# Kernel optimization log

Measured on AMD Instinct MI355X. Metric: run time of the kernel, lower is better.

The kernel has to match this reference:

```python
import jax, jax.numpy as jnp
import numpy as np
from jax import lax

B, L, P, CIN, N, HD, PH, K = 2048, 96, 96, 8, 64, 64, 8, 3
DIM_C = CIN * N  # 512


def _silu(x):
    return x * jax.nn.sigmoid(x)


def _lin(x, w, b):
    return x @ w.T + b


def setup_inputs() -> dict:
    key = jax.random.key(0)
    ks = iter(jax.random.split(key, 64))

    def w(shape):
        fan_in = shape[-1]
        return (jax.random.normal(next(ks), shape, jnp.float32) / np.sqrt(fan_in)).astype(jnp.float32)

    inp = {"x": jax.random.normal(next(ks), (B, L, CIN), jnp.float32)}
    # x_proj: 5 Linears (enc_in->h, h->h, h->h, h->h, h->N), SiLU between (dropout=eval/identity)
    inp["xp_w0"] = w((HD, CIN)); inp["xp_b0"] = jnp.zeros((HD,), jnp.float32)
    inp["xp_w1"] = w((HD, HD));  inp["xp_b1"] = jnp.zeros((HD,), jnp.float32)
    inp["xp_w2"] = w((HD, HD));  inp["xp_b2"] = jnp.zeros((HD,), jnp.float32)
    inp["xp_w3"] = w((HD, HD));  inp["xp_b3"] = jnp.zeros((HD,), jnp.float32)
    inp["xp_w4"] = w((N, HD));   inp["xp_b4"] = jnp.zeros((N,), jnp.float32)
    # x_proj_: Linear(N,h), SiLU, Linear(h,N)
    inp["xpp_w0"] = w((HD, N)); inp["xpp_b0"] = jnp.zeros((HD,), jnp.float32)
    inp["xpp_w1"] = w((N, HD)); inp["xpp_b1"] = jnp.zeros((N,), jnp.float32)
    # depthwise dilated Conv1d: weight (N, 1, K)
    inp["conv_w"] = w((N, 1, K)); inp["conv_b"] = jnp.zeros((N,), jnp.float32)
    inp["span_A"] = jnp.asarray(0.1, jnp.float32)
    # compress: Linear(N*L, PH)
    inp["comp_w"] = w((PH, N * L)); inp["comp_b"] = jnp.zeros((PH,), jnp.float32)
    # a_ode.net: Linear(PH,h), SiLU, Linear(h,PH), Tanh
    inp["net_w0"] = w((HD, PH)); inp["net_b0"] = jnp.zeros((HD,), jnp.float32)
    inp["net_w1"] = w((PH, HD)); inp["net_b1"] = jnp.zeros((PH,), jnp.float32)
    # lat2out: Linear(PH,8), SiLU, Linear(8,N)
    inp["lo_w0"] = w((8, PH)); inp["lo_b0"] = jnp.zeros((8,), jnp.float32)
    inp["lo_w1"] = w((N, 8));  inp["lo_b1"] = jnp.zeros((N,), jnp.float32)
    # lat2out_c: Linear(PH,8), SiLU, Linear(8, CIN*N)
    inp["lc_w0"] = w((8, PH));     inp["lc_b0"] = jnp.zeros((8,), jnp.float32)
    inp["lc_w1"] = w((DIM_C, 8));  inp["lc_b1"] = jnp.zeros((DIM_C,), jnp.float32)
    # lat2out_z: Linear(N,N), SiLU, Linear(N, CIN)
    inp["lz_w0"] = w((N, N));   inp["lz_b0"] = jnp.zeros((N,), jnp.float32)
    inp["lz_w1"] = w((CIN, N)); inp["lz_b1"] = jnp.zeros((CIN,), jnp.float32)
    return inp


def reference(x, xp_w0, xp_b0, xp_w1, xp_b1, xp_w2, xp_b2, xp_w3, xp_b3, xp_w4, xp_b4,
              xpp_w0, xpp_b0, xpp_w1, xpp_b1, conv_w, conv_b, span_A, comp_w, comp_b,
              net_w0, net_b0, net_w1, net_b1, lo_w0, lo_b0, lo_w1, lo_b1,
              lc_w0, lc_b0, lc_w1, lc_b1, lz_w0, lz_b0, lz_w1, lz_b1):
    Bsz = x.shape[0]

    def x_proj(t):
        h = _silu(_lin(t, xp_w0, xp_b0))
        h = _silu(_lin(h, xp_w1, xp_b1))
        h = _silu(_lin(h, xp_w2, xp_b2))
        h = _silu(_lin(h, xp_w3, xp_b3))
        return _lin(h, xp_w4, xp_b4)

    x_old = x_proj(x[:, :L])                       # (B, L, N)
    hist = x_old.transpose(0, 2, 1)                # (B, N, L)
    pad = (K - 1) * 2                              # 4
    conv = lax.conv_general_dilated(
        hist, conv_w, window_strides=(1,), padding=[(pad, pad)],
        rhs_dilation=(2,), dimension_numbers=("NCH", "OIH", "NCH"),
        feature_group_count=N) + conv_b[None, :, None]
    hist = _silu(conv)[:, :, -L:]                  # (B, N, L)
    hist_f = hist.transpose(0, 2, 1).reshape(Bsz, L * N)
    vector_F = _lin(hist_f, comp_w, comp_b)        # (B, PH)

    a0 = vector_F
    z0 = x_proj(x[:, L - 1])                       # (B, N)

    # Householder matrix H = I - 2 v v^T with v = normalize(x_proj_(z0))
    v = _lin(_silu(_lin(z0, xpp_w0, xpp_b0)), xpp_w1, xpp_b1)
    v = v / (jnp.linalg.norm(v, axis=-1, keepdims=True) + 1e-8)
    Hh = jnp.eye(N, dtype=x.dtype)[None] - 2.0 * v[:, :, None] * v[:, None, :]  # (B,N,N)

    dt = jnp.clip(span_A, 1e-8, 7.0)               # uniform Euler step size
    s0 = jnp.concatenate([a0, z0], axis=-1)        # (B, PH+N)

    def step(s, _):
        a = s[:, :PH]
        z = s[:, PH:]
        da = jnp.tanh(_lin(_silu(_lin(a, net_w0, net_b0)), net_w1, net_b1))  # (B,PH)
        d = _lin(_silu(_lin(a, lo_w0, lo_b0)), lo_w1, lo_b1)                 # (B,N)
        # dz = H^T diag(d) H z   (fused; avoids materializing A_mat)
        Hz = jnp.einsum('bjk,bk->bj', Hh, z)
        dz = jnp.einsum('bj,bji->bi', d * Hz, Hh)
        s_new = s + dt * jnp.concatenate([da, dz], axis=-1)
        return s_new, s_new

    _, sol = lax.scan(step, s0, None, length=P)    # (P, B, PH+N) == sol[1:]

    c_traj = sol[:, :, :PH]                        # (P, B, PH)
    z_traj = sol[:, :, PH:]                        # (P, B, N)

    C = _lin(_silu(_lin(c_traj, lc_w0, lc_b0)), lc_w1, lc_b1)  # (P, B, CIN*N)
    C = C.reshape(P, Bsz, CIN, N)
    y_hat_c = jnp.einsum('pbcn,pbn->pbc', C, z_traj)           # (P, B, CIN)
    added_z = _lin(_silu(_lin(z_traj, lz_w0, lz_b0)), lz_w1, lz_b1)
    x_pred = (y_hat_c + added_z).transpose(1, 0, 2)            # (B, P, CIN)

    x_rec = x[:, :L, :]
    return (x_rec, x_pred)
```

## Files before the change

kernel.cpp:

```cpp
#include <hip/hip_runtime.h>
#include <cstdint>
#include <cstddef>

#define BB 2048
#define LL 96
#define PP 96
#define NN 64
#define HSTRIDE 68
#define RSTR 84

typedef __attribute__((ext_vector_type(8))) short short8;
typedef __attribute__((ext_vector_type(4))) float f32x4;

union U4S8 { uint4 u; short8 s; };

__device__ __forceinline__ float siluf(float x) {
  return x * __builtin_amdgcn_rcpf(1.0f + __expf(-x));
}
__device__ __forceinline__ float tanhf_fast(float x) {
  return 1.0f - 2.0f * __builtin_amdgcn_rcpf(1.0f + __expf(2.0f * x));
}
__device__ __forceinline__ float rlane(float x, int l) {
  return __int_as_float(__builtin_amdgcn_readlane(__float_as_int(x), l));
}

__device__ __forceinline__ uint32_t packsplit(float f) {
  uint32_t b = __float_as_uint(f);
  uint32_t h = b & 0xFFFF0000u;
  float r = f - __uint_as_float(h);
  return h | (__float_as_uint(r) >> 16);
}
__device__ __forceinline__ void splitpack2(float f0, float f1, uint32_t& dhi, uint32_t& dlo) {
  uint32_t b0 = __float_as_uint(f0), b1 = __float_as_uint(f1);
  uint32_t h0 = b0 & 0xFFFF0000u, h1 = b1 & 0xFFFF0000u;
  float r0 = f0 - __uint_as_float(h0), r1 = f1 - __uint_as_float(h1);
  dhi = (h0 >> 16) | h1;
  dlo = (__float_as_uint(r0) >> 16) | (__float_as_uint(r1) & 0xFFFF0000u);
}
__device__ __forceinline__ void unpack2(uint32_t p0, uint32_t p1, uint32_t& dhi, uint32_t& dlo) {
  dhi = (p0 >> 16) | (p1 & 0xFFFF0000u);
  dlo = (p0 & 0xFFFFu) | (p1 << 16);
}
__device__ __forceinline__ void readfrag(const uint32_t* p, short8& hi, short8& lo) {
  uint4 pa = *(const uint4*)p;
  uint4 pb = *(const uint4*)(p + 4);
  U4S8 h, l;
  unpack2(pa.x, pa.y, h.u.x, l.u.x);
  unpack2(pa.z, pa.w, h.u.y, l.u.y);
  unpack2(pb.x, pb.y, h.u.z, l.u.z);
  unpack2(pb.z, pb.w, h.u.w, l.u.w);
  hi = h.s; lo = l.s;
}
__device__ __forceinline__ f32x4 mm_split(f32x4 acc, const short8* Ah, const short8* Al,
                                          const short8* Bh, const short8* Bl) {
  acc = __builtin_amdgcn_mfma_f32_16x16x32_bf16(Ah[0], Bh[0], acc, 0, 0, 0);
  acc = __builtin_amdgcn_mfma_f32_16x16x32_bf16(Ah[1], Bh[1], acc, 0, 0, 0);
  acc = __builtin_amdgcn_mfma_f32_16x16x32_bf16(Al[0], Bh[0], acc, 0, 0, 0);
  acc = __builtin_amdgcn_mfma_f32_16x16x32_bf16(Al[1], Bh[1], acc, 0, 0, 0);
  acc = __builtin_amdgcn_mfma_f32_16x16x32_bf16(Ah[0], Bl[0], acc, 0, 0, 0);
  acc = __builtin_amdgcn_mfma_f32_16x16x32_bf16(Ah[1], Bl[1], acc, 0, 0, 0);
  return acc;
}

__global__ __launch_bounds__(256, 2) void k_xproj(
    const float* __restrict__ x,
    const float* __restrict__ w0, const float* __restrict__ b0,
    const float* __restrict__ w1, const float* __restrict__ b1,
    const float* __restrict__ w2, const float* __restrict__ b2,
    const float* __restrict__ w3, const float* __restrict__ b3,
    const float* __restrict__ w4, const float* __restrict__ b4,
    float* __restrict__ x_old, float* __restrict__ out)
{
  __shared__ uint32_t hbuf[128 * HSTRIDE];
  __shared__ uint32_t wbuf[64 * HSTRIDE];
  __shared__ float bs[320];

  int tid = threadIdx.x;
  int wave = tid >> 6, lane = tid & 63;
  int quad = lane >> 4, m16 = lane & 15;
  size_t tokBase = (size_t)blockIdx.x * 128;

  {
    size_t e = tokBase * 8 + (size_t)tid * 4;
    *(float4*)(out + e) = *(const float4*)(x + e);
  }
  if (tid < 64) {
    bs[tid]       = b0[tid];
    bs[64 + tid]  = b1[tid];
    bs[128 + tid] = b2[tid];
    bs[192 + tid] = b3[tid];
    bs[256 + tid] = b4[tid];
  }
  __syncthreads();

  short8 A0h[2], A0l[2];
  #pragma unroll
  for (int mt = 0; mt < 2; ++mt) {
    U4S8 h, l;
    h.u = make_uint4(0, 0, 0, 0); l.u = make_uint4(0, 0, 0, 0);
    if (quad == 0) {
      const float* xp = x + (tokBase + wave * 32 + mt * 16 + m16) * 8;
      float4 xa = *(const float4*)xp;
      float4 xb = *(const float4*)(xp + 4);
      splitpack2(xa.x, xa.y, h.u.x, l.u.x);
      splitpack2(xa.z, xa.w, h.u.y, l.u.y);
      splitpack2(xb.x, xb.y, h.u.z, l.u.z);
      splitpack2(xb.z, xb.w, h.u.w, l.u.w);
    }
    A0h[mt] = h.s; A0l[mt] = l.s;
  }
  short8 B0h[4], B0l[4];
  #pragma unroll
  for (int nt = 0; nt < 4; ++nt) {
    U4S8 h, l;
    h.u = make_uint4(0, 0, 0, 0); l.u = make_uint4(0, 0, 0, 0);
    if (quad == 0) {
      const float* wp = w0 + (nt * 16 + m16) * 8;
      float4 wa = *(const float4*)wp;
      float4 wb = *(const float4*)(wp + 4);
      splitpack2(wa.x, wa.y, h.u.x, l.u.x);
      splitpack2(wa.z, wa.w, h.u.y, l.u.y);
      splitpack2(wb.x, wb.y, h.u.z, l.u.z);
      splitpack2(wb.z, wb.w, h.u.w, l.u.w);
    }
    B0h[nt] = h.s; B0l[nt] = l.s;
  }
  {
    f32x4 acc[2][4];
    #pragma unroll
    for (int mt = 0; mt < 2; ++mt)
      #pragma unroll
      for (int nt = 0; nt < 4; ++nt) {
        float bv = bs[nt * 16 + m16];
        acc[mt][nt] = (f32x4){bv, bv, bv, bv};
      }
    #pragma unroll
    for (int mt = 0; mt < 2; ++mt)
      #pragma unroll
      for (int nt = 0; nt < 4; ++nt)
        acc[mt][nt] = __builtin_amdgcn_mfma_f32_16x16x32_bf16(A0h[mt], B0h[nt], acc[mt][nt], 0, 0, 0);
    #pragma unroll
    for (int mt = 0; mt < 2; ++mt)
      #pragma unroll
      for (int nt = 0; nt < 4; ++nt)
        acc[mt][nt] = __builtin_amdgcn_mfma_f32_16x16x32_bf16(A0l[mt], B0h[nt], acc[mt][nt], 0, 0, 0);
    #pragma unroll
    for (int mt = 0; mt < 2; ++mt)
      #pragma unroll
      for (int nt = 0; nt < 4; ++nt)
        acc[mt][nt] = __builtin_amdgcn_mfma_f32_16x16x32_bf16(A0h[mt], B0l[nt], acc[mt][nt], 0, 0, 0);
    #pragma unroll
    for (int mt = 0; mt < 2; ++mt)
      #pragma unroll
      for (int nt = 0; nt < 4; ++nt)
        #pragma unroll
        for (int r = 0; r < 4; ++r) {
          float s = siluf(acc[mt][nt][r]);
          hbuf[(wave * 32 + mt * 16 + quad * 4 + r) * HSTRIDE + nt * 16 + m16] = packsplit(s);
        }
  }

  const float* Ws[4] = {w1, w2, w3, w4};
  #pragma unroll 1
  for (int lyr = 0; lyr < 4; ++lyr) {
    const float* w = Ws[lyr];
    #pragma unroll
    for (int i = 0; i < 4; ++i) {
      int e4 = i * 256 + tid;
      int o = e4 >> 4, k = (e4 & 15) << 2;
      float4 wv = ((const float4*)w)[e4];
      *(uint4*)(wbuf + o * HSTRIDE + k) =
          make_uint4(packsplit(wv.x), packsplit(wv.y), packsplit(wv.z), packsplit(wv.w));
    }
    __syncthreads();
    short8 Bh[8], Bl[8];
    #pragma unroll
    for (int nt = 0; nt < 4; ++nt)
      #pragma unroll
      for (int ks = 0; ks < 2; ++ks)
        readfrag(wbuf + (nt * 16 + m16) * HSTRIDE + ks * 32 + quad * 8, Bh[nt * 2 + ks], Bl[nt * 2 + ks]);
    short8 Ah[4], Al[4];
    #pragma unroll
    for (int mt = 0; mt < 2; ++mt)
      #pragma unroll
      for (int ks = 0; ks < 2; ++ks)
        readfrag(hbuf + (wave * 32 + mt * 16 + m16) * HSTRIDE + ks * 32 + quad * 8, Ah[mt * 2 + ks], Al[mt * 2 + ks]);
    __syncthreads();

    f32x4 acc[2][4];
    #pragma unroll
    for (int mt = 0; mt < 2; ++mt)
      #pragma unroll
      for (int nt = 0; nt < 4; ++nt) {
        float bv = bs[(lyr + 1) * 64 + nt * 16 + m16];
        acc[mt][nt] = (f32x4){bv, bv, bv, bv};
      }
    #pragma unroll
    for (int ks = 0; ks < 2; ++ks)
      #pragma unroll
      for (int mt = 0; mt < 2; ++mt)
        #pragma unroll
        for (int nt = 0; nt < 4; ++nt)
          acc[mt][nt] = __builtin_amdgcn_mfma_f32_16x16x32_bf16(Ah[mt * 2 + ks], Bh[nt * 2 + ks], acc[mt][nt], 0, 0, 0);
    #pragma unroll
    for (int ks = 0; ks < 2; ++ks)
      #pragma unroll
      for (int mt = 0; mt < 2; ++mt)
        #pragma unroll
        for (int nt = 0; nt < 4; ++nt)
          acc[mt][nt] = __builtin_amdgcn_mfma_f32_16x16x32_bf16(Al[mt * 2 + ks], Bh[nt * 2 + ks], acc[mt][nt], 0, 0, 0);
    #pragma unroll
    for (int ks = 0; ks < 2; ++ks)
      #pragma unroll
      for (int mt = 0; mt < 2; ++mt)
        #pragma unroll
        for (int nt = 0; nt < 4; ++nt)
          acc[mt][nt] = __builtin_amdgcn_mfma_f32_16x16x32_bf16(Ah[mt * 2 + ks], Bl[nt * 2 + ks], acc[mt][nt], 0, 0, 0);

    if (lyr < 3) {
      #pragma unroll
      for (int mt = 0; mt < 2; ++mt)
        #pragma unroll
        for (int nt = 0; nt < 4; ++nt)
          #pragma unroll
          for (int r = 0; r < 4; ++r) {
            float s = siluf(acc[mt][nt][r]);
            hbuf[(wave * 32 + mt * 16 + quad * 4 + r) * HSTRIDE + nt * 16 + m16] = packsplit(s);
          }
    } else {
      #pragma unroll
      for (int mt = 0; mt < 2; ++mt)
        #pragma unroll
        for (int nt = 0; nt < 4; ++nt)
          #pragma unroll
          for (int r = 0; r < 4; ++r) {
            size_t t = tokBase + wave * 32 + mt * 16 + quad * 4 + r;
            x_old[t * 64 + nt * 16 + m16] = acc[mt][nt][r];
          }
    }
  }
}

__global__ __launch_bounds__(256) void k_hist(
    const float* __restrict__ x_old,
    const float* __restrict__ conv_w, const float* __restrict__ conv_b,
    const float* __restrict__ comp_w, const float* __restrict__ comp_b,
    const float* __restrict__ xw0, const float* __restrict__ xb0,
    const float* __restrict__ xw1, const float* __restrict__ xb1,
    float* __restrict__ a0_o, float* __restrict__ v_o, float* __restrict__ z0_o)
{
  __shared__ float xo[LL * NN];
  __shared__ float red[32];
  __shared__ float hbuf[64];
  int b = blockIdx.x, tid = threadIdx.x;
  const float* src = x_old + (size_t)b * (LL * NN);
  #pragma unroll
  for (int i = 0; i < 6; ++i) {
    int e = (i * 256 + tid) * 4;
    *(float4*)(xo + e) = *(const float4*)(src + e);
  }
  __syncthreads();
  int c = tid & 63;
  float cw0 = conv_w[c * 3], cw1 = conv_w[c * 3 + 1], cw2 = conv_w[c * 3 + 2];
  float cb = conv_b[c];
  float acc[8];
  #pragma unroll
  for (int q = 0; q < 8; ++q) acc[q] = 0.f;
  #pragma unroll 1
  for (int j = 0; j < 24; ++j) {
    int e = j * 256 + tid;
    int t = e >> 6;
    float s = xo[t * 64 + c] * cw0 + cb;
    if (t + 2 < LL) s += xo[(t + 2) * 64 + c] * cw1;
    if (t + 4 < LL) s += xo[(t + 4) * 64 + c] * cw2;
    float hv = siluf(s);
    #pragma unroll
    for (int q = 0; q < 8; ++q) acc[q] += hv * comp_w[q * 6144 + e];
  }
  #pragma unroll
  for (int off = 32; off >= 1; off >>= 1) {
    #pragma unroll
    for (int q = 0; q < 8; ++q) acc[q] += __shfl_xor(acc[q], off, 64);
  }
  int wave = tid >> 6, lane = tid & 63;
  if (lane < 8) {
    float sel = acc[0];
    #pragma unroll
    for (int q = 1; q < 8; ++q) sel = (lane == q) ? acc[q] : sel;
    red[wave * 8 + lane] = sel;
  }
  __syncthreads();
  if (tid < 8)
    a0_o[b * 8 + tid] = red[tid] + red[8 + tid] + red[16 + tid] + red[24 + tid] + comp_b[tid];
  if (tid < 64) {
    float a2 = xb0[tid];
    #pragma unroll 8
    for (int k = 0; k < 64; ++k) a2 += xw0[tid * 64 + k] * xo[6080 + k];
    hbuf[tid] = siluf(a2);
  }
  __syncthreads();
  float vr = 0.f;
  if (tid < 64) {
    vr = xb1[tid];
    #pragma unroll 8
    for (int k = 0; k < 64; ++k) vr += xw1[tid * 64 + k] * hbuf[k];
  }
  float s2 = vr * vr;
  #pragma unroll
  for (int off = 32; off >= 1; off >>= 1) s2 += __shfl_xor(s2, off, 64);
  if (tid < 64) {
    float nrm = sqrtf(s2) + 1e-8f;
    v_o[b * 64 + tid] = vr / nrm;
    z0_o[b * 64 + tid] = xo[6080 + tid];
  }
}

__global__ __launch_bounds__(256) void k_scan(
    const float* __restrict__ a0_i, const float* __restrict__ v_i, const float* __restrict__ z0_i,
    const float* __restrict__ nw0, const float* __restrict__ nb0_p,
    const float* __restrict__ nw1, const float* __restrict__ nb1_p,
    const float* __restrict__ lw0, const float* __restrict__ lb0_p,
    const float* __restrict__ lw1, const float* __restrict__ lb1_p,
    const float* __restrict__ spanA, float* __restrict__ atraj, float* __restrict__ ztraj)
{
  int lane = threadIdx.x & 63;
  int b = blockIdx.x * 4 + (threadIdx.x >> 6);
  float dt = fminf(fmaxf(spanA[0], 1e-8f), 7.0f);
  int i8 = lane & 7;
  float w0r[8], w1r[8], g0r[8], d1r[8];
  #pragma unroll
  for (int i = 0; i < 8; ++i) w0r[i] = nw0[lane * 8 + i];
  #pragma unroll
  for (int i = 0; i < 8; ++i) w1r[i] = nw1[i * 64 + lane];
  #pragma unroll
  for (int i = 0; i < 8; ++i) g0r[i] = lw0[i8 * 8 + i];
  #pragma unroll
  for (int i = 0; i < 8; ++i) d1r[i] = lw1[lane * 8 + i];
  float nb0 = nb0_p[lane];
  float nb1o = nb1_p[i8];
  float lb0o = lb0_p[i8];
  float lb1 = lb1_p[lane];
  float v = v_i[b * 64 + lane];
  float z = z0_i[b * 64 + lane];
  float a_own = a0_i[b * 8 + i8];
  float t0 = v * z;
  #pragma unroll
  for (int off = 32; off >= 1; off >>= 1) t0 += __shfl_xor(t0, off, 64);
  float w = z - 2.0f * t0 * v;
  float a_s[8];
  #pragma unroll
  for (int i = 0; i < 8; ++i) a_s[i] = rlane(a_own, i);

  float* ab = atraj + (size_t)b * (PP * 8);
  float* zb = ztraj + (size_t)b * (PP * NN);
  #pragma unroll 1
  for (int p = 0; p < PP; ++p) {
    float h = nb0;
    #pragma unroll
    for (int i = 0; i < 8; ++i) h += w0r[i] * a_s[i];
    h = siluf(h);
    float pr[8];
    #pragma unroll
    for (int i = 0; i < 8; ++i) pr[i] = w1r[i] * h;
    #pragma unroll
    for (int off = 1; off <= 4; off <<= 1) {
      #pragma unroll
      for (int i = 0; i < 8; ++i) pr[i] += __shfl_xor(pr[i], off, 64);
    }
    float ps = pr[0];
    #pragma unroll
    for (int i = 1; i < 8; ++i) ps = (i8 == i) ? pr[i] : ps;
    ps += __shfl_xor(ps, 8, 64);
    ps += __shfl_xor(ps, 16, 64);
    ps += __shfl_xor(ps, 32, 64);
    float da_own = tanhf_fast(ps + nb1o);
    float ga = lb0o;
    #pragma unroll
    for (int i = 0; i < 8; ++i) ga += g0r[i] * a_s[i];
    float g_own = siluf(ga);
    float d = lb1;
    #pragma unroll
    for (int j = 0; j < 8; ++j) d += d1r[j] * rlane(g_own, j);
    a_own += dt * da_own;
    #pragma unroll
    for (int i = 0; i < 8; ++i) a_s[i] = rlane(a_own, i);
    w *= (1.0f + dt * d);
    float t1 = v * w;
    #pragma unroll
    for (int off = 32; off >= 1; off >>= 1) t1 += __shfl_xor(t1, off, 64);
    float zv = w - 2.0f * t1 * v;
    if (lane < 8) ab[p * 8 + lane] = a_own;
    zb[p * 64 + lane] = zv;
  }
}

__global__ __launch_bounds__(256, 2) void k_post(
    const float* __restrict__ atraj, const float* __restrict__ ztraj,
    const float* __restrict__ cw0, const float* __restrict__ cb0,
    const float* __restrict__ cw1, const float* __restrict__ cb1,
    const float* __restrict__ zw0, const float* __restrict__ zb0,
    const float* __restrict__ zw1, const float* __restrict__ zb1,
    float* __restrict__ out)
{
  __shared__ uint32_t zbuf[64 * HSTRIDE];
  __shared__ uint32_t wbuf[80 * HSTRIDE];
  __shared__ float    resbuf[64 * RSTR];
  __shared__ float    cw0s[64];
  __shared__ float    cb0s[8];
  __shared__ float    zb0s[64];
  __shared__ float    zb1s[8];

  int tid = threadIdx.x;
  int wave = tid >> 6, lane = tid & 63;
  int quad = lane >> 4, m16 = lane & 15;
  size_t tokBase = (size_t)blockIdx.x * 64;

  #pragma unroll
  for (int i = 0; i < 4; ++i) {
    int e4 = i * 256 + tid;
    int t = e4 >> 4, k = (e4 & 15) << 2;
    float4 zv = *(const float4*)(ztraj + (tokBase + t) * 64 + k);
    *(uint4*)(zbuf + t * HSTRIDE + k) =
        make_uint4(packsplit(zv.x), packsplit(zv.y), packsplit(zv.z), packsplit(zv.w));
  }
  #pragma unroll
  for (int i = 0; i < 20; ++i) {
    int e = i * 256 + tid;
    int o = e >> 6, k = e & 63;
    float wv;
    if (o < 64)       wv = cw1[(((o >> 3) * 64 + k) << 3) + (o & 7)];
    else if (o < 72)  wv = cb1[(o - 64) * 64 + k];
    else              wv = 0.f;
    wbuf[o * HSTRIDE + k] = packsplit(wv);
  }
  if (tid < 64) cw0s[tid] = cw0[tid];
  if (tid < 8)  cb0s[tid] = cb0[tid];
  if (tid < 64) zb0s[tid] = zb0[tid];
  if (tid < 8)  zb1s[tid] = zb1[tid];
  __syncthreads();

  short8 Ah[2], Al[2];
  readfrag(zbuf + (wave * 16 + m16) * HSTRIDE + quad * 8,      Ah[0], Al[0]);
  readfrag(zbuf + (wave * 16 + m16) * HSTRIDE + 32 + quad * 8, Ah[1], Al[1]);

  #pragma unroll
  for (int nt = 0; nt < 5; ++nt) {
    short8 Bh[2], Bl[2];
    readfrag(wbuf + (nt * 16 + m16) * HSTRIDE + quad * 8,      Bh[0], Bl[0]);
    readfrag(wbuf + (nt * 16 + m16) * HSTRIDE + 32 + quad * 8, Bh[1], Bl[1]);
    f32x4 acc = (f32x4){0.f, 0.f, 0.f, 0.f};
    acc = mm_split(acc, Ah, Al, Bh, Bl);
    int o = nt * 16 + m16;
    if (o < 72) {
      #pragma unroll
      for (int r = 0; r < 4; ++r)
        resbuf[(wave * 16 + quad * 4 + r) * RSTR + o] = acc[r];
    }
  }
  __syncthreads();

  #pragma unroll
  for (int i = 0; i < 16; ++i) {
    int e = i * 256 + tid;
    int o = e >> 6, k = e & 63;
    wbuf[o * HSTRIDE + k] = packsplit(zw0[o * 64 + k]);
  }
  __syncthreads();

  #pragma unroll
  for (int nt = 0; nt < 4; ++nt) {
    short8 Bh[2], Bl[2];
    readfrag(wbuf + (nt * 16 + m16) * HSTRIDE + quad * 8,      Bh[0], Bl[0]);
    readfrag(wbuf + (nt * 16 + m16) * HSTRIDE + 32 + quad * 8, Bh[1], Bl[1]);
    f32x4 acc = (f32x4){0.f, 0.f, 0.f, 0.f};
    acc = mm_split(acc, Ah, Al, Bh, Bl);
    int m = nt * 16 + m16;
    float zb = zb0s[m];
    #pragma unroll
    for (int r = 0; r < 4; ++r) {
      float e = siluf(acc[r] + zb);
      zbuf[(wave * 16 + quad * 4 + r) * HSTRIDE + m] = packsplit(e);
    }
  }
  __syncthreads();

  #pragma unroll
  for (int i = 0; i < 4; ++i) {
    int e = i * 256 + tid;
    int o = e >> 6, k = e & 63;
    wbuf[o * HSTRIDE + k] = (o < 8) ? packsplit(zw1[o * 64 + k]) : 0u;
  }
  __syncthreads();

  {
    short8 Eh[2], El[2];
    readfrag(zbuf + (wave * 16 + m16) * HSTRIDE + quad * 8,      Eh[0], El[0]);
    readfrag(zbuf + (wave * 16 + m16) * HSTRIDE + 32 + quad * 8, Eh[1], El[1]);
    short8 Bh[2], Bl[2];
    readfrag(wbuf + m16 * HSTRIDE + quad * 8,      Bh[0], Bl[0]);
    readfrag(wbuf + m16 * HSTRIDE + 32 + quad * 8, Bh[1], Bl[1]);
    f32x4 acc = (f32x4){0.f, 0.f, 0.f, 0.f};
    acc = mm_split(acc, Eh, El, Bh, Bl);
    if (m16 < 8) {
      float zb = zb1s[m16];
      #pragma unroll
      for (int r = 0; r < 4; ++r)
        resbuf[(wave * 16 + quad * 4 + r) * RSTR + 72 + m16] = acc[r] + zb;
    }
  }
  __syncthreads();

  if (tid < 64) {
    size_t idx = tokBase + tid;
    const float* ap = atraj + idx * 8;
    float4 a0v = *(const float4*)ap;
    float4 a1v = *(const float4*)(ap + 4);
    float a[8] = {a0v.x, a0v.y, a0v.z, a0v.w, a1v.x, a1v.y, a1v.z, a1v.w};
    float g2[8];
    #pragma unroll
    for (int j = 0; j < 8; ++j) {
      float t = cb0s[j];
      #pragma unroll
      for (int i = 0; i < 8; ++i) t += cw0s[j * 8 + i] * a[i];
      g2[j] = siluf(t);
    }
    const float* rr = resbuf + tid * RSTR;
    float yc[8];
    #pragma unroll
    for (int c = 0; c < 8; ++c) {
      float y = rr[64 + c] + rr[72 + c];
      #pragma unroll
      for (int j = 0; j < 8; ++j) y += rr[c * 8 + j] * g2[j];
      yc[c] = y;
    }
    float* op = out + (size_t)(BB * LL * 8) + idx * 8;
    *(float4*)op       = make_float4(yc[0], yc[1], yc[2], yc[3]);
    *(float4*)(op + 4) = make_float4(yc[4], yc[5], yc[6], yc[7]);
  }
}

extern "C" void kernel_launch(void* const* d_in, const int* in_sizes, int n_in,
                              void* d_out, int out_size, void* d_ws, size_t ws_size,
                              hipStream_t stream) {
  const float* x      = (const float*)d_in[0];
  const float* xp_w0  = (const float*)d_in[1];
  const float* xp_b0  = (const float*)d_in[2];
  const float* xp_w1  = (const float*)d_in[3];
  const float* xp_b1  = (const float*)d_in[4];
  const float* xp_w2  = (const float*)d_in[5];
  const float* xp_b2  = (const float*)d_in[6];
  const float* xp_w3  = (const float*)d_in[7];
  const float* xp_b3  = (const float*)d_in[8];
  const float* xp_w4  = (const float*)d_in[9];
  const float* xp_b4  = (const float*)d_in[10];
  const float* xpp_w0 = (const float*)d_in[11];
  const float* xpp_b0 = (const float*)d_in[12];
  const float* xpp_w1 = (const float*)d_in[13];
  const float* xpp_b1 = (const float*)d_in[14];
  const float* conv_w = (const float*)d_in[15];
  const float* conv_b = (const float*)d_in[16];
  const float* span_A = (const float*)d_in[17];
  const float* comp_w = (const float*)d_in[18];
  const float* comp_b = (const float*)d_in[19];
  const float* net_w0 = (const float*)d_in[20];
  const float* net_b0 = (const float*)d_in[21];
  const float* net_w1 = (const float*)d_in[22];
  const float* net_b1 = (const float*)d_in[23];
  const float* lo_w0  = (const float*)d_in[24];
  const float* lo_b0  = (const float*)d_in[25];
  const float* lo_w1  = (const float*)d_in[26];
  const float* lo_b1  = (const float*)d_in[27];
  const float* lc_w0  = (const float*)d_in[28];
  const float* lc_b0  = (const float*)d_in[29];
  const float* lc_w1  = (const float*)d_in[30];
  const float* lc_b1  = (const float*)d_in[31];
  const float* lz_w0  = (const float*)d_in[32];
  const float* lz_b0  = (const float*)d_in[33];
  const float* lz_w1  = (const float*)d_in[34];
  const float* lz_b1  = (const float*)d_in[35];

  float* ws    = (float*)d_ws;
  float* x_old = ws;
  float* ztraj = ws;
  float* atraj = ws + 12582912;
  float* a0    = ws + 14155776;
  float* vv    = a0 + 2048 * 8;
  float* z0    = vv + 2048 * 64;
  float* out   = (float*)d_out;

  hipLaunchKernelGGL(k_xproj, dim3(1536), dim3(256), 0, stream,
                     x, xp_w0, xp_b0, xp_w1, xp_b1, xp_w2, xp_b2, xp_w3, xp_b3,
                     xp_w4, xp_b4, x_old, out);
  hipLaunchKernelGGL(k_hist, dim3(2048), dim3(256), 0, stream,
                     x_old, conv_w, conv_b, comp_w, comp_b,
                     xpp_w0, xpp_b0, xpp_w1, xpp_b1, a0, vv, z0);
  hipLaunchKernelGGL(k_scan, dim3(512), dim3(256), 0, stream,
                     a0, vv, z0, net_w0, net_b0, net_w1, net_b1,
                     lo_w0, lo_b0, lo_w1, lo_b1, span_A, atraj, ztraj);
  hipLaunchKernelGGL(k_post, dim3(3072), dim3(256), 0, stream,
                     atraj, ztraj, lc_w0, lc_b0, lc_w1, lc_b1,
                     lz_w0, lz_b0, lz_w1, lz_b1, out);
}
```

Measured before the change: 361.4 us.

## Pre-split z trajectory in scan, preload all post weights, LDS-based da reduction

The scan kernel now writes z trajectory values already packed into the hi/lo split format, and computes the net_w1 product by staging h in shared memory instead of a shuffle-heavy 8-way reduction. The post kernel reads A fragments directly from global memory, loads all of its weight matrices into one larger LDS buffer up front (removing several barriers and reload phases), and spreads the final output computation over all 256 threads. The result buffer stride also changes. The aim is fewer syncs, less conversion work and fewer shuffles. The cost is more LDS per block, which may reduce occupancy.

```diff
diff --git a/kernel.cpp b/kernel.cpp
--- a/kernel.cpp
+++ b/kernel.cpp
@@ -7,7 +7,7 @@
 #define PP 96
 #define NN 64
 #define HSTRIDE 68
-#define RSTR 84
+#define RSTR 81
 
 typedef __attribute__((ext_vector_type(8))) short short8;
 typedef __attribute__((ext_vector_type(4))) float f32x4;
@@ -321,17 +321,23 @@
     const float* __restrict__ nw1, const float* __restrict__ nb1_p,
     const float* __restrict__ lw0, const float* __restrict__ lb0_p,
     const float* __restrict__ lw1, const float* __restrict__ lb1_p,
-    const float* __restrict__ spanA, float* __restrict__ atraj, float* __restrict__ ztraj)
+    const float* __restrict__ spanA, float* __restrict__ atraj, uint32_t* __restrict__ ztraj)
 {
-  int lane = threadIdx.x & 63;
-  int b = blockIdx.x * 4 + (threadIdx.x >> 6);
+  __shared__ float hshm[4 * 72];
+  int tid = threadIdx.x;
+  int lane = tid & 63;
+  int wv = tid >> 6;
+  int b = blockIdx.x * 4 + wv;
   float dt = fminf(fmaxf(spanA[0], 1e-8f), 7.0f);
   int i8 = lane & 7;
-  float w0r[8], w1r[8], g0r[8], d1r[8];
+  int oct = lane >> 3;
+  float* hs = hshm + wv * 72;
+
+  float w0r[8], w1L[8], g0r[8], d1r[8];
   #pragma unroll
   for (int i = 0; i < 8; ++i) w0r[i] = nw0[lane * 8 + i];
   #pragma unroll
-  for (int i = 0; i < 8; ++i) w1r[i] = nw1[i * 64 + lane];
+  for (int j = 0; j < 8; ++j) w1L[j] = nw1[i8 * 64 + oct * 8 + j];
   #pragma unroll
   for (int i = 0; i < 8; ++i) g0r[i] = lw0[i8 * 8 + i];
   #pragma unroll
@@ -352,28 +358,22 @@
   for (int i = 0; i < 8; ++i) a_s[i] = rlane(a_own, i);
 
   float* ab = atraj + (size_t)b * (PP * 8);
-  float* zb = ztraj + (size_t)b * (PP * NN);
+  uint32_t* zb = ztraj + (size_t)b * (PP * NN);
   #pragma unroll 1
   for (int p = 0; p < PP; ++p) {
     float h = nb0;
     #pragma unroll
     for (int i = 0; i < 8; ++i) h += w0r[i] * a_s[i];
     h = siluf(h);
-    float pr[8];
-    #pragma unroll
-    for (int i = 0; i < 8; ++i) pr[i] = w1r[i] * h;
-    #pragma unroll
-    for (int off = 1; off <= 4; off <<= 1) {
-      #pragma unroll
-      for (int i = 0; i < 8; ++i) pr[i] += __shfl_xor(pr[i], off, 64);
-    }
-    float ps = pr[0];
-    #pragma unroll
-    for (int i = 1; i < 8; ++i) ps = (i8 == i) ? pr[i] : ps;
-    ps += __shfl_xor(ps, 8, 64);
-    ps += __shfl_xor(ps, 16, 64);
-    ps += __shfl_xor(ps, 32, 64);
-    float da_own = tanhf_fast(ps + nb1o);
+    hs[lane] = h;
+    float4 h0 = *(const float4*)(hs + oct * 8);
+    float4 h1 = *(const float4*)(hs + oct * 8 + 4);
+    float psum = w1L[0] * h0.x + w1L[1] * h0.y + w1L[2] * h0.z + w1L[3] * h0.w
+               + w1L[4] * h1.x + w1L[5] * h1.y + w1L[6] * h1.z + w1L[7] * h1.w;
+    psum += __shfl_xor(psum, 8, 64);
+    psum += __shfl_xor(psum, 16, 64);
+    psum += __shfl_xor(psum, 32, 64);
+    float da_own = tanhf_fast(psum + nb1o);
     float ga = lb0o;
     #pragma unroll
     for (int i = 0; i < 8; ++i) ga += g0r[i] * a_s[i];
@@ -390,20 +390,20 @@
     for (int off = 32; off >= 1; off >>= 1) t1 += __shfl_xor(t1, off, 64);
     float zv = w - 2.0f * t1 * v;
     if (lane < 8) ab[p * 8 + lane] = a_own;
-    zb[p * 64 + lane] = zv;
+    zb[p * 64 + lane] = packsplit(zv);
   }
 }
 
 __global__ __launch_bounds__(256, 2) void k_post(
-    const float* __restrict__ atraj, const float* __restrict__ ztraj,
+    const float* __restrict__ atraj, const uint32_t* __restrict__ ztraj,
     const float* __restrict__ cw0, const float* __restrict__ cb0,
     const float* __restrict__ cw1, const float* __restrict__ cb1,
     const float* __restrict__ zw0, const float* __restrict__ zb0,
     const float* __restrict__ zw1, const float* __restrict__ zb1,
     float* __restrict__ out)
 {
-  __shared__ uint32_t zbuf[64 * HSTRIDE];
-  __shared__ uint32_t wbuf[80 * HSTRIDE];
+  __shared__ uint32_t wbuf[144 * HSTRIDE];
+  __shared__ uint32_t ebuf[64 * HSTRIDE];
   __shared__ float    resbuf[64 * RSTR];
   __shared__ float    cw0s[64];
   __shared__ float    cb0s[8];
@@ -416,21 +416,14 @@
   size_t tokBase = (size_t)blockIdx.x * 64;
 
   #pragma unroll
-  for (int i = 0; i < 4; ++i) {
-    int e4 = i * 256 + tid;
-    int t = e4 >> 4, k = (e4 & 15) << 2;
-    float4 zv = *(const float4*)(ztraj + (tokBase + t) * 64 + k);
-    *(uint4*)(zbuf + t * HSTRIDE + k) =
-        make_uint4(packsplit(zv.x), packsplit(zv.y), packsplit(zv.z), packsplit(zv.w));
-  }
-  #pragma unroll
-  for (int i = 0; i < 20; ++i) {
+  for (int i = 0; i < 36; ++i) {
     int e = i * 256 + tid;
     int o = e >> 6, k = e & 63;
     float wv;
     if (o < 64)       wv = cw1[(((o >> 3) * 64 + k) << 3) + (o & 7)];
     else if (o < 72)  wv = cb1[(o - 64) * 64 + k];
-    else              wv = 0.f;
+    else if (o < 136) wv = zw0[(o - 72) * 64 + k];
+    else              wv = zw1[(o - 136) * 64 + k];
     wbuf[o * HSTRIDE + k] = packsplit(wv);
   }
   if (tid < 64) cw0s[tid] = cw0[tid];
@@ -439,9 +432,10 @@
   if (tid < 8)  zb1s[tid] = zb1[tid];
   __syncthreads();
 
+  const uint32_t* zp = ztraj + (tokBase + wave * 16 + m16) * 64;
   short8 Ah[2], Al[2];
-  readfrag(zbuf + (wave * 16 + m16) * HSTRIDE + quad * 8,      Ah[0], Al[0]);
-  readfrag(zbuf + (wave * 16 + m16) * HSTRIDE + 32 + quad * 8, Ah[1], Al[1]);
+  readfrag(zp + quad * 8,      Ah[0], Al[0]);
+  readfrag(zp + 32 + quad * 8, Ah[1], Al[1]);
 
   #pragma unroll
   for (int nt = 0; nt < 5; ++nt) {
@@ -457,61 +451,45 @@
         resbuf[(wave * 16 + quad * 4 + r) * RSTR + o] = acc[r];
     }
   }
-  __syncthreads();
-
-  #pragma unroll
-  for (int i = 0; i < 16; ++i) {
-    int e = i * 256 + tid;
-    int o = e >> 6, k = e & 63;
-    wbuf[o * HSTRIDE + k] = packsplit(zw0[o * 64 + k]);
-  }
-  __syncthreads();
 
   #pragma unroll
   for (int nt = 0; nt < 4; ++nt) {
     short8 Bh[2], Bl[2];
-    readfrag(wbuf + (nt * 16 + m16) * HSTRIDE + quad * 8,      Bh[0], Bl[0]);
-    readfrag(wbuf + (nt * 16 + m16) * HSTRIDE + 32 + quad * 8, Bh[1], Bl[1]);
+    readfrag(wbuf + (72 + nt * 16 + m16) * HSTRIDE + quad * 8,      Bh[0], Bl[0]);
+    readfrag(wbuf + (72 + nt * 16 + m16) * HSTRIDE + 32 + quad * 8, Bh[1], Bl[1]);
     f32x4 acc = (f32x4){0.f, 0.f, 0.f, 0.f};
     acc = mm_split(acc, Ah, Al, Bh, Bl);
     int m = nt * 16 + m16;
-    float zb = zb0s[m];
+    float zbv = zb0s[m];
     #pragma unroll
     for (int r = 0; r < 4; ++r) {
-      float e = siluf(acc[r] + zb);
-      zbuf[(wave * 16 + quad * 4 + r) * HSTRIDE + m] = packsplit(e);
-    }
-  }
-  __syncthreads();
-
-  #pragma unroll
-  for (int i = 0; i < 4; ++i) {
-    int e = i * 256 + tid;
-    int o = e >> 6, k = e & 63;
-    wbuf[o * HSTRIDE + k] = (o < 8) ? packsplit(zw1[o * 64 + k]) : 0u;
-  }
-  __syncthreads();
+      float e = siluf(acc[r] + zbv);
+      ebuf[(wave * 16 + quad * 4 + r) * HSTRIDE + m] = packsplit(e);
+    }
+  }
 
   {
     short8 Eh[2], El[2];
-    readfrag(zbuf + (wave * 16 + m16) * HSTRIDE + quad * 8,      Eh[0], El[0]);
-    readfrag(zbuf + (wave * 16 + m16) * HSTRIDE + 32 + quad * 8, Eh[1], El[1]);
+    readfrag(ebuf + (wave * 16 + m16) * HSTRIDE + quad * 8,      Eh[0], El[0]);
+    readfrag(ebuf + (wave * 16 + m16) * HSTRIDE + 32 + quad * 8, Eh[1], El[1]);
     short8 Bh[2], Bl[2];
-    readfrag(wbuf + m16 * HSTRIDE + quad * 8,      Bh[0], Bl[0]);
-    readfrag(wbuf + m16 * HSTRIDE + 32 + quad * 8, Bh[1], Bl[1]);
+    int brow = 136 + (m16 & 7);
+    readfrag(wbuf + brow * HSTRIDE + quad * 8,      Bh[0], Bl[0]);
+    readfrag(wbuf + brow * HSTRIDE + 32 + quad * 8, Bh[1], Bl[1]);
     f32x4 acc = (f32x4){0.f, 0.f, 0.f, 0.f};
     acc = mm_split(acc, Eh, El, Bh, Bl);
     if (m16 < 8) {
-      float zb = zb1s[m16];
+      float zbv = zb1s[m16];
       #pragma unroll
       for (int r = 0; r < 4; ++r)
-        resbuf[(wave * 16 + quad * 4 + r) * RSTR + 72 + m16] = acc[r] + zb;
+        resbuf[(wave * 16 + quad * 4 + r) * RSTR + 72 + m16] = acc[r] + zbv;
     }
   }
   __syncthreads();
 
-  if (tid < 64) {
-    size_t idx = tokBase + tid;
+  {
+    int t = tid & 63, cg = tid >> 6;
+    size_t idx = tokBase + t;
     const float* ap = atraj + idx * 8;
     float4 a0v = *(const float4*)ap;
     float4 a1v = *(const float4*)(ap + 4);
@@ -519,23 +497,22 @@
     float g2[8];
     #pragma unroll
     for (int j = 0; j < 8; ++j) {
-      float t = cb0s[j];
-      #pragma unroll
-      for (int i = 0; i < 8; ++i) t += cw0s[j * 8 + i] * a[i];
-      g2[j] = siluf(t);
-    }
-    const float* rr = resbuf + tid * RSTR;
-    float yc[8];
-    #pragma unroll
-    for (int c = 0; c < 8; ++c) {
-      float y = rr[64 + c] + rr[72 + c];
-      #pragma unroll
-      for (int j = 0; j < 8; ++j) y += rr[c * 8 + j] * g2[j];
-      yc[c] = y;
-    }
-    float* op = out + (size_t)(BB * LL * 8) + idx * 8;
-    *(float4*)op       = make_float4(yc[0], yc[1], yc[2], yc[3]);
-    *(float4*)(op + 4) = make_float4(yc[4], yc[5], yc[6], yc[7]);
+      float tt = cb0s[j];
+      #pragma unroll
+      for (int i = 0; i < 8; ++i) tt += cw0s[j * 8 + i] * a[i];
+      g2[j] = siluf(tt);
+    }
+    const float* rr = resbuf + t * RSTR;
+    int c0 = cg * 2;
+    float y0 = rr[64 + c0] + rr[72 + c0];
+    float y1 = rr[64 + c0 + 1] + rr[72 + c0 + 1];
+    #pragma unroll
+    for (int j = 0; j < 8; ++j) {
+      y0 += rr[c0 * 8 + j] * g2[j];
+      y1 += rr[(c0 + 1) * 8 + j] * g2[j];
+    }
+    float* op = out + (size_t)(BB * LL * 8) + idx * 8 + c0;
+    *(float2*)op = make_float2(y0, y1);
   }
 }
 
@@ -579,14 +556,14 @@
   const float* lz_w1  = (const float*)d_in[34];
   const float* lz_b1  = (const float*)d_in[35];
 
-  float* ws    = (float*)d_ws;
-  float* x_old = ws;
-  float* ztraj = ws;
-  float* atraj = ws + 12582912;
-  float* a0    = ws + 14155776;
-  float* vv    = a0 + 2048 * 8;
-  float* z0    = vv + 2048 * 64;
-  float* out   = (float*)d_out;
+  float*    ws    = (float*)d_ws;
+  float*    x_old = ws;
+  uint32_t* ztraj = (uint32_t*)ws;
+  float*    atraj = ws + 12582912;
+  float*    a0    = ws + 14155776;
+  float*    vv    = a0 + 2048 * 8;
+  float*    z0    = vv + 2048 * 64;
+  float*    out   = (float*)d_out;
 
   hipLaunchKernelGGL(k_xproj, dim3(1536), dim3(256), 0, stream,
                      x, xp_w0, xp_b0, xp_w1, xp_b1, xp_w2, xp_b2, xp_w3, xp_b3,
```

Result: faster. 323.5 us (-10.5%).
